# Optimization experiments

Hardware: AMD Instinct MI355X
Metric: run time of the kernel (lower is better)

The kernel has to match this reference:

```python
import jax, jax.numpy as jnp
import numpy as np

D_MODEL = 1024
EXPAND = 2
D_INNER = EXPAND * D_MODEL      # 2048
D_STATE = 2
D_CONV = 4
DT_RANK = (D_MODEL + 15) // 16  # 64
BATCH, SEQ = 2, 4096
LN_EPS = 1e-5


def setup_inputs() -> dict:
    key = jax.random.key(0)
    ks = jax.random.split(key, 16)
    s = 0.02
    inp = {
        "x":       jax.random.normal(ks[0], (BATCH, SEQ, D_MODEL), jnp.float32),
        # Mamba params (torch Linear convention: W is [out, in])
        "w_in":    jax.random.normal(ks[1], (2 * D_INNER, D_MODEL), jnp.float32) * s,
        "conv_w":  jax.random.normal(ks[2], (D_INNER, 1, D_CONV), jnp.float32) * s,
        "conv_b":  jnp.zeros((D_INNER,), jnp.float32),
        "w_xproj": jax.random.normal(ks[3], (DT_RANK + 2 * D_STATE, D_INNER), jnp.float32) * s,
        "w_dt":    jax.random.normal(ks[4], (D_INNER, DT_RANK), jnp.float32) * s,
        "b_dt":    jax.random.normal(ks[5], (D_INNER,), jnp.float32) * s - 4.0,  # softplus -> small dt
        "a_log":   jnp.log(jnp.broadcast_to(jnp.arange(1, D_STATE + 1, dtype=jnp.float32), (D_INNER, D_STATE))),
        "d_skip":  jnp.ones((D_INNER,), jnp.float32),
        "w_out":   jax.random.normal(ks[6], (D_MODEL, D_INNER), jnp.float32) * s,
        # LayerNorms
        "ln1_g":   jnp.ones((D_MODEL,), jnp.float32),
        "ln1_b":   jnp.zeros((D_MODEL,), jnp.float32),
        "ln2_g":   jnp.ones((D_MODEL,), jnp.float32),
        "ln2_b":   jnp.zeros((D_MODEL,), jnp.float32),
        # FFN (Linear d->d, ReLU, Linear d->d; dropout inactive at eval)
        "ffn_w1":  jax.random.normal(ks[7], (D_MODEL, D_MODEL), jnp.float32) * s,
        "ffn_b1":  jnp.zeros((D_MODEL,), jnp.float32),
        "ffn_w2":  jax.random.normal(ks[8], (D_MODEL, D_MODEL), jnp.float32) * s,
        "ffn_b2":  jnp.zeros((D_MODEL,), jnp.float32),
    }
    return inp


def _ln(x, g, b):
    mu = x.mean(-1, keepdims=True)
    v = ((x - mu) ** 2).mean(-1, keepdims=True)
    return (x - mu) * jax.lax.rsqrt(v + LN_EPS) * g + b


def _mamba(x, w_in, conv_w, conv_b, w_xproj, w_dt, b_dt, a_log, d_skip, w_out):
    Bsz = x.shape[0]
    xz = x @ w_in.T                      # (B,L,2*D_INNER)
    xp, z = jnp.split(xz, 2, axis=-1)
    # depthwise causal conv over time
    xc = jnp.transpose(xp, (0, 2, 1))    # (B,D,L)
    xc = jax.lax.conv_general_dilated(
        xc, conv_w, window_strides=(1,), padding=[(D_CONV - 1, 0)],
        feature_group_count=D_INNER)
    xc = xc + conv_b[None, :, None]
    xp = jax.nn.silu(jnp.transpose(xc, (0, 2, 1)))   # (B,L,D)
    # input-dependent SSM params
    x_dbl = xp @ w_xproj.T               # (B,L,DT_RANK+2N)
    dt, Bm, Cm = jnp.split(x_dbl, [DT_RANK, DT_RANK + D_STATE], axis=-1)
    dt = jax.nn.softplus(dt @ w_dt.T + b_dt)          # (B,L,D)
    A = -jnp.exp(a_log)                  # (D,N)
    dA = jnp.exp(dt[..., None] * A)                  # (B,L,D,N)
    dBu = dt[..., None] * Bm[:, :, None, :] * xp[..., None]  # (B,L,D,N)

    def step(h, inp):
        da, dbu, c = inp                 # (B,D,N),(B,D,N),(B,N)
        h = da * h + dbu
        y = jnp.einsum('bdn,bn->bd', h, c)
        return h, y

    h0 = jnp.zeros((Bsz, D_INNER, D_STATE), x.dtype)
    _, ys = jax.lax.scan(step, h0, (jnp.swapaxes(dA, 0, 1),
                                    jnp.swapaxes(dBu, 0, 1),
                                    jnp.swapaxes(Cm, 0, 1)))
    y = jnp.swapaxes(ys, 0, 1)           # (B,L,D)
    y = (y + d_skip * xp) * jax.nn.silu(z)
    return y @ w_out.T                   # (B,L,d_model)


def reference(x, w_in, conv_w, conv_b, w_xproj, w_dt, b_dt, a_log, d_skip, w_out,
              ln1_g, ln1_b, ln2_g, ln2_b, ffn_w1, ffn_b1, ffn_w2, ffn_b2):
    h = x + _mamba(_ln(x, ln1_g, ln1_b), w_in, conv_w, conv_b, w_xproj,
                   w_dt, b_dt, a_log, d_skip, w_out)
    f = _ln(h, ln2_g, ln2_b)
    f = jax.nn.relu(f @ ffn_w1.T + ffn_b1) @ ffn_w2.T + ffn_b2
    return h + f
```

## Files before the change

kernel.cpp:

```cpp
#include <hip/hip_runtime.h>

typedef unsigned short u16;
typedef __bf16 bf16x8 __attribute__((ext_vector_type(8)));
typedef float f32x4 __attribute__((ext_vector_type(4)));
typedef float f32x2 __attribute__((ext_vector_type(2)));
typedef u16 u16x4 __attribute__((ext_vector_type(4)));
typedef u16 u16x8 __attribute__((ext_vector_type(8)));

#define SEQ   4096
#define DM    1024
#define DI    2048
#define NTOK  8192
#define NXP   68
#define DTR   64
#define NCH   4096
#define CHUNK 32
#define NCHK  128

__device__ __forceinline__ float bf2f(u16 v) {
  union { unsigned u; float f; } x; x.u = ((unsigned)v) << 16; return x.f;
}
__device__ __forceinline__ u16 f2bf(float f) {
  unsigned u = __float_as_uint(f);
  return (u16)((u + 0x7FFFu + ((u >> 16) & 1u)) >> 16);
}

__device__ __forceinline__ void g2l16(const u16* g, u16* l) {
  __builtin_amdgcn_global_load_lds(
      (const __attribute__((address_space(1))) unsigned int*)g,
      (__attribute__((address_space(3))) unsigned int*)l, 16, 0, 0);
}

__global__ __launch_bounds__(256)
void detect_kernel(const u16* __restrict__ x, int* __restrict__ flag)
{
  __shared__ int tot;
  if (threadIdx.x == 0) tot = 0;
  __syncthreads();
  int cnt = 0;
  for (int i = threadIdx.x; i < 4096; i += 256) {
    const int e = (x[2 * i] >> 7) & 0xFF;
    if (e > 167) cnt++;
  }
  atomicAdd(&tot, cnt);
  __syncthreads();
  if (threadIdx.x == 0) flag[0] = (tot >= 8) ? 1 : 0;
}

#define NW0 4194304
#define NW1  139264
#define NW2  131072
#define NW3 2097152
#define NW4 1048576
#define NW5 1048576
#define NBB 4228
__global__ __launch_bounds__(256)
void convert_all(const float* __restrict__ s0, const float* __restrict__ s1,
                 const float* __restrict__ s2, const float* __restrict__ s3,
                 const float* __restrict__ s4, const float* __restrict__ s5,
                 u16* __restrict__ d0, u16* __restrict__ d1, u16* __restrict__ d2,
                 u16* __restrict__ d3, u16* __restrict__ d4, u16* __restrict__ d5,
                 const void* t0, const void* t1, const void* t2, const void* t3,
                 const void* t4, const void* t5, const void* t6, const void* t7,
                 const void* t8, const void* t9, const void* t10,
                 u16* __restrict__ dsm, const int* __restrict__ flag)
{
  if (blockIdx.x >= NBB) {
    const int i = (blockIdx.x - NBB) * 256 + threadIdx.x;
    if (i >= 24576) return;
    const void* src; int off; int dsti = i;
    if      (i < 8192)  { src = t0;  off = i;
                          dsti = (off & 3) * DI + (off >> 2); }
    else if (i < 10240) { src = t1;  off = i - 8192; }
    else if (i < 12288) { src = t2;  off = i - 10240; }
    else if (i < 16384) { src = t3;  off = i - 12288; }
    else if (i < 18432) { src = t4;  off = i - 16384; }
    else if (i < 19456) { src = t5;  off = i - 18432; }
    else if (i < 20480) { src = t6;  off = i - 19456; }
    else if (i < 21504) { src = t7;  off = i - 20480; }
    else if (i < 22528) { src = t8;  off = i - 21504; }
    else if (i < 23552) { src = t9;  off = i - 22528; }
    else                { src = t10; off = i - 23552; }
    dsm[dsti] = (*flag) ? f2bf(((const float*)src)[off]) : ((const u16*)src)[off];
    return;
  }
  if (*flag == 0) return;
  long e = ((long)blockIdx.x * 256 + threadIdx.x) * 8;
  const long c1 = NW0, c2 = c1 + NW1, c3 = c2 + NW2, c4 = c3 + NW3,
             c5 = c4 + NW4, c6 = c5 + NW5;
  if (e >= c6) return;
  const float* s; u16* d;
  if      (e < c1) { s = s0;          d = d0; }
  else if (e < c2) { s = s1; e -= c1; d = d1; }
  else if (e < c3) { s = s2; e -= c2; d = d2; }
  else if (e < c4) { s = s3; e -= c3; d = d3; }
  else if (e < c5) { s = s4; e -= c4; d = d4; }
  else             { s = s5; e -= c5; d = d5; }
  f32x4 a = *(const f32x4*)(s + e);
  f32x4 b = *(const f32x4*)(s + e + 4);
  u16x8 o;
#pragma unroll
  for (int k = 0; k < 4; ++k) { o[k] = f2bf(a[k]); o[4 + k] = f2bf(b[k]); }
  *(u16x8*)(d + e) = o;
}

template<int MODE>
__global__ __launch_bounds__(256)
void ln_kernel(const void* __restrict__ xin, const u16* __restrict__ gw,
               const u16* __restrict__ bw, u16* __restrict__ outp,
               const int* __restrict__ flag)
{
  const int tid = threadIdx.x;
  const int sub = tid >> 7;
  const int col0 = (tid & 127) * 8;
  const int row = blockIdx.x * 2 + sub;
  const bool isf32 = (MODE == 0) ? (*flag != 0) : false;
  float v[8];
  if (isf32) {
    const float* xf = (const float*)xin + (size_t)row * DM + col0;
    f32x4 a = *(const f32x4*)xf, b2 = *(const f32x4*)(xf + 4);
#pragma unroll
    for (int k = 0; k < 4; ++k) { v[k] = a[k]; v[4 + k] = b2[k]; }
  } else {
    u16x8 xb = *(const u16x8*)((const u16*)xin + (size_t)row * DM + col0);
#pragma unroll
    for (int k = 0; k < 8; ++k) v[k] = bf2f(xb[k]);
  }
  float s = 0.f, s2 = 0.f;
#pragma unroll
  for (int k = 0; k < 8; ++k) { s += v[k]; s2 += v[k] * v[k]; }
#pragma unroll
  for (int off = 32; off > 0; off >>= 1) {
    s  += __shfl_down(s,  off);
    s2 += __shfl_down(s2, off);
  }
  __shared__ float red[4], red2[4];
  __shared__ f32x2 stat[2];
  const int wv = tid >> 6;
  if ((tid & 63) == 0) { red[wv] = s; red2[wv] = s2; }
  __syncthreads();
  if ((tid & 127) == 0) {
    float ts = red[sub * 2] + red[sub * 2 + 1];
    float t2 = red2[sub * 2] + red2[sub * 2 + 1];
    float mu = ts * (1.f / DM);
    float var = t2 * (1.f / DM) - mu * mu;
    stat[sub] = f32x2{mu, rsqrtf(var + 1e-5f)};
  }
  __syncthreads();
  const float mu = stat[sub][0], rs = stat[sub][1];
  u16x8 gv = *(const u16x8*)(gw + col0), bv = *(const u16x8*)(bw + col0);
  u16x8 o;
#pragma unroll
  for (int k = 0; k < 8; ++k)
    o[k] = f2bf((v[k] - mu) * rs * bf2f(gv[k]) + bf2f(bv[k]));
  *(u16x8*)(outp + (size_t)row * DM + col0) = o;
}

template<int EPI, int LNBX>
__global__ __launch_bounds__(256, 2)
void gemm_kernel(const u16* __restrict__ A, const u16* __restrict__ Bc,
                 const u16* __restrict__ Braw,
                 int M, int N, int K,
                 const u16* __restrict__ bias, const u16* __restrict__ addbf,
                 const float* __restrict__ addf, const int* __restrict__ dtflag,
                 void* __restrict__ Cp, void* __restrict__ Cp2)
{
  __shared__ __align__(16) u16 sA[2][128 * 32];
  __shared__ __align__(16) u16 sB[2][128 * 32];
  const int fl = *dtflag;
  const u16* __restrict__ B = fl ? Bc : Braw;
  const int tid = threadIdx.x;
  const int b = blockIdx.x;
  const int xcd = b & 7;
  const int kk = b >> 3;
  const int bx = kk & ((1 << LNBX) - 1);
  const int by = xcd * 8 + (kk >> LNBX);
  const int m0 = by * 128;
  const int n0 = bx * 128;
  const int lane = tid & 63;
  const int wv = tid >> 6;
  const int wm = (wv & 1) * 64;
  const int wn = (wv >> 1) * 64;
  const int r = lane & 15;
  const int q = lane >> 4;
  const int rsw = (r >> 1) & 3;

  const int pr = lane >> 2;
  const int kc = (lane & 3) ^ ((pr >> 1) & 3);
  const int pk = kc * 8;
  u16* lA0[2] = { &sA[0][(wv * 2 + 0) * 512], &sA[1][(wv * 2 + 0) * 512] };
  u16* lA1[2] = { &sA[0][(wv * 2 + 1) * 512], &sA[1][(wv * 2 + 1) * 512] };
  u16* lB0[2] = { &sB[0][(wv * 2 + 0) * 512], &sB[1][(wv * 2 + 0) * 512] };
  u16* lB1[2] = { &sB[0][(wv * 2 + 1) * 512], &sB[1][(wv * 2 + 1) * 512] };
  const u16* gA0 = A + (size_t)(m0 + wv * 32 + pr) * K + pk;
  const u16* gA1 = gA0 + (size_t)16 * K;
  const u16* gB0 = B + (size_t)(n0 + wv * 32 + pr) * K + pk;
  const u16* gB1 = gB0 + (size_t)16 * K;

  f32x4 acc[4][4];
#pragma unroll
  for (int i = 0; i < 4; ++i)
#pragma unroll
    for (int j = 0; j < 4; ++j)
#pragma unroll
      for (int t = 0; t < 4; ++t) acc[i][j][t] = 0.f;

  g2l16(gA0, lA0[0]); g2l16(gA1, lA1[0]);
  g2l16(gB0, lB0[0]); g2l16(gB1, lB1[0]);

  const int nk = K >> 5;
  for (int kt = 0; kt < nk; ++kt) {
    const int cur = kt & 1;
    __syncthreads();
    bf16x8 af[4], bfr[4];
#pragma unroll
    for (int i = 0; i < 4; ++i)
      af[i] = *reinterpret_cast<const bf16x8*>(
          &sA[cur][(wm + i * 16 + r) * 32 + (q ^ rsw) * 8]);
#pragma unroll
    for (int j = 0; j < 4; ++j)
      bfr[j] = *reinterpret_cast<const bf16x8*>(
          &sB[cur][(wn + j * 16 + r) * 32 + (q ^ rsw) * 8]);
    if (kt + 1 < nk) {
      gA0 += 32; gA1 += 32; gB0 += 32; gB1 += 32;
      g2l16(gA0, lA0[cur ^ 1]); g2l16(gA1, lA1[cur ^ 1]);
      g2l16(gB0, lB0[cur ^ 1]); g2l16(gB1, lB1[cur ^ 1]);
    }
#pragma unroll
    for (int i = 0; i < 4; ++i)
#pragma unroll
      for (int j = 0; j < 4; ++j)
        acc[i][j] = __builtin_amdgcn_mfma_f32_16x16x32_bf16(af[i], bfr[j], acc[i][j], 0, 0, 0);
  }

  __syncthreads();
  float* ep = (wv < 2) ? ((float*)&sA[0][0] + wv * 2048)
                       : ((float*)&sB[0][0] + (wv - 2) * 2048);
  const int r2 = lane >> 2;
  const int ccol = ((lane & 3) ^ (r2 & 3)) * 16;
  u16* C6 = nullptr; int c6off = 0;
  if (EPI == 6) { C6 = (n0 < DI) ? (u16*)Cp : (u16*)Cp2; c6off = (n0 < DI) ? 0 : DI; }

#pragma unroll
  for (int i = 0; i < 4; ++i) {
#pragma unroll
    for (int j = 0; j < 4; ++j)
#pragma unroll
      for (int t = 0; t < 4; ++t)
        ep[(q * 4 + t) * 68 + j * 16 + r] = acc[i][j][t];
    f32x4 w0 = *(const f32x4*)&ep[r2 * 68 + ccol + 0];
    f32x4 w1 = *(const f32x4*)&ep[r2 * 68 + ccol + 4];
    f32x4 w2 = *(const f32x4*)&ep[r2 * 68 + ccol + 8];
    f32x4 w3 = *(const f32x4*)&ep[r2 * 68 + ccol + 12];
    float vv[16];
#pragma unroll
    for (int k = 0; k < 4; ++k) {
      vv[k] = w0[k]; vv[4 + k] = w1[k]; vv[8 + k] = w2[k]; vv[12 + k] = w3[k];
    }
    const int row = m0 + wm + i * 16 + r2;
    const int colg = n0 + wn + ccol;
    if (EPI == 6) {
      u16x8 o0, o1;
#pragma unroll
      for (int k = 0; k < 8; ++k) { o0[k] = f2bf(vv[k]); o1[k] = f2bf(vv[8 + k]); }
      const size_t cb6 = (size_t)row * DI + (colg - c6off);
      *(u16x8*)&C6[cb6] = o0;
      *(u16x8*)&C6[cb6 + 8] = o1;
    } else {
      const size_t idx = (size_t)row * N + colg;
      if (EPI == 1) {
        u16x8 o0, o1;
#pragma unroll
        for (int k = 0; k < 8; ++k) { o0[k] = f2bf(vv[k]); o1[k] = f2bf(vv[8 + k]); }
        *(u16x8*)&((u16*)Cp)[idx] = o0;
        *(u16x8*)&((u16*)Cp)[idx + 8] = o1;
      } else if (EPI == 2) {
        u16x8 b0 = *(const u16x8*)&bias[colg];
        u16x8 b1 = *(const u16x8*)&bias[colg + 8];
        u16x8 o0, o1;
#pragma unroll
        for (int k = 0; k < 8; ++k) {
          float v0 = vv[k] + bf2f(b0[k]);
          float v1 = vv[8 + k] + bf2f(b1[k]);
          v0 = (v0 > 15.f) ? v0 : __logf(1.f + __expf(v0));
          v1 = (v1 > 15.f) ? v1 : __logf(1.f + __expf(v1));
          o0[k] = f2bf(v0); o1[k] = f2bf(v1);
        }
        *(u16x8*)&((u16*)Cp)[idx] = o0;
        *(u16x8*)&((u16*)Cp)[idx + 8] = o1;
      } else if (EPI == 3) {
        float ax[16];
        if (fl) {
          f32x4 a0 = *(const f32x4*)&addf[idx];
          f32x4 a1 = *(const f32x4*)&addf[idx + 4];
          f32x4 a2 = *(const f32x4*)&addf[idx + 8];
          f32x4 a3 = *(const f32x4*)&addf[idx + 12];
#pragma unroll
          for (int k = 0; k < 4; ++k) {
            ax[k] = a0[k]; ax[4 + k] = a1[k]; ax[8 + k] = a2[k]; ax[12 + k] = a3[k];
          }
        } else {
          u16x8 a0 = *(const u16x8*)&addbf[idx];
          u16x8 a1 = *(const u16x8*)&addbf[idx + 8];
#pragma unroll
          for (int k = 0; k < 8; ++k) { ax[k] = bf2f(a0[k]); ax[8 + k] = bf2f(a1[k]); }
        }
        u16x8 o0, o1;
#pragma unroll
        for (int k = 0; k < 8; ++k) {
          o0[k] = f2bf(vv[k] + ax[k]); o1[k] = f2bf(vv[8 + k] + ax[8 + k]);
        }
        *(u16x8*)&((u16*)Cp)[idx] = o0;
        *(u16x8*)&((u16*)Cp)[idx + 8] = o1;
      } else if (EPI == 4) {
        u16x8 b0 = *(const u16x8*)&bias[colg];
        u16x8 b1 = *(const u16x8*)&bias[colg + 8];
        u16x8 o0, o1;
#pragma unroll
        for (int k = 0; k < 8; ++k) {
          o0[k] = f2bf(fmaxf(vv[k] + bf2f(b0[k]), 0.f));
          o1[k] = f2bf(fmaxf(vv[8 + k] + bf2f(b1[k]), 0.f));
        }
        *(u16x8*)&((u16*)Cp)[idx] = o0;
        *(u16x8*)&((u16*)Cp)[idx + 8] = o1;
      } else {
        u16x8 b0 = *(const u16x8*)&bias[colg];
        u16x8 b1 = *(const u16x8*)&bias[colg + 8];
        u16x8 a0 = *(const u16x8*)&addbf[idx];
        u16x8 a1 = *(const u16x8*)&addbf[idx + 8];
        float r0[8], r1[8];
#pragma unroll
        for (int k = 0; k < 8; ++k) {
          r0[k] = vv[k] + bf2f(b0[k]) + bf2f(a0[k]);
          r1[k] = vv[8 + k] + bf2f(b1[k]) + bf2f(a1[k]);
        }
        if (fl) {
          f32x4 f0, f1, f2, f3;
#pragma unroll
          for (int k = 0; k < 4; ++k) { f0[k] = r0[k]; f1[k] = r0[4 + k]; f2[k] = r1[k]; f3[k] = r1[4 + k]; }
          *(f32x4*)&((float*)Cp)[idx] = f0;
          *(f32x4*)&((float*)Cp)[idx + 4] = f1;
          *(f32x4*)&((float*)Cp)[idx + 8] = f2;
          *(f32x4*)&((float*)Cp)[idx + 12] = f3;
        } else {
          u16x8 o0, o1;
#pragma unroll
          for (int k = 0; k < 8; ++k) { o0[k] = f2bf(r0[k]); o1[k] = f2bf(r1[k]); }
          *(u16x8*)&((u16*)Cp)[idx] = o0;
          *(u16x8*)&((u16*)Cp)[idx + 8] = o1;
        }
      }
    }
  }
}

__global__ __launch_bounds__(256, 2)
void xproj_splitk(const u16* __restrict__ A, const u16* __restrict__ Bc,
                  const u16* __restrict__ Braw, const int* __restrict__ dtflag,
                  float* __restrict__ part)
{
  __shared__ __align__(16) u16 sA[2][128 * 32];
  __shared__ __align__(16) u16 sB[2][128 * 32];
  const int fl = *dtflag;
  const u16* __restrict__ B = fl ? Bc : Braw;
  const int tid = threadIdx.x;
  const int kz = blockIdx.x;
  const int m0 = blockIdx.y * 128;
  const int kbase = kz * 256;
  const int lane = tid & 63;
  const int wv = tid >> 6;
  const int wm = (wv & 1) * 64;
  const int wn = (wv >> 1) * 64;
  const int r = lane & 15;
  const int q = lane >> 4;
  const int rsw = (r >> 1) & 3;
  const int pr = lane >> 2;
  const int kc = (lane & 3) ^ ((pr >> 1) & 3);
  const int pk = kc * 8;

  u16* lA0[2] = { &sA[0][(wv * 2 + 0) * 512], &sA[1][(wv * 2 + 0) * 512] };
  u16* lA1[2] = { &sA[0][(wv * 2 + 1) * 512], &sA[1][(wv * 2 + 1) * 512] };
  u16* lB0[2] = { &sB[0][(wv * 2 + 0) * 512], &sB[1][(wv * 2 + 0) * 512] };
  u16* lB1[2] = { &sB[0][(wv * 2 + 1) * 512], &sB[1][(wv * 2 + 1) * 512] };
  int br0 = wv * 32 + pr;      if (br0 > 67) br0 = 67;
  int br1 = wv * 32 + 16 + pr; if (br1 > 67) br1 = 67;
  const u16* gA0 = A + (size_t)(m0 + wv * 32 + pr) * DI + kbase + pk;
  const u16* gA1 = gA0 + (size_t)16 * DI;
  const u16* gB0 = B + (size_t)br0 * DI + kbase + pk;
  const u16* gB1 = B + (size_t)br1 * DI + kbase + pk;

  f32x4 acc[4][4];
#pragma unroll
  for (int i = 0; i < 4; ++i)
#pragma unroll
    for (int j = 0; j < 4; ++j)
#pragma unroll
      for (int t = 0; t < 4; ++t) acc[i][j][t] = 0.f;

  g2l16(gA0, lA0[0]); g2l16(gA1, lA1[0]);
  g2l16(gB0, lB0[0]); g2l16(gB1, lB1[0]);

  for (int kt = 0; kt < 8; ++kt) {
    const int cur = kt & 1;
    __syncthreads();
    bf16x8 af[4], bfr[4];
#pragma unroll
    for (int i = 0; i < 4; ++i)
      af[i] = *reinterpret_cast<const bf16x8*>(
          &sA[cur][(wm + i * 16 + r) * 32 + (q ^ rsw) * 8]);
#pragma unroll
    for (int j = 0; j < 4; ++j)
      bfr[j] = *reinterpret_cast<const bf16x8*>(
          &sB[cur][(wn + j * 16 + r) * 32 + (q ^ rsw) * 8]);
    if (kt + 1 < 8) {
      gA0 += 32; gA1 += 32; gB0 += 32; gB1 += 32;
      g2l16(gA0, lA0[cur ^ 1]); g2l16(gA1, lA1[cur ^ 1]);
      g2l16(gB0, lB0[cur ^ 1]); g2l16(gB1, lB1[cur ^ 1]);
    }
#pragma unroll
    for (int i = 0; i < 4; ++i)
#pragma unroll
      for (int j = 0; j < 4; ++j)
        acc[i][j] = __builtin_amdgcn_mfma_f32_16x16x32_bf16(af[i], bfr[j], acc[i][j], 0, 0, 0);
  }

#pragma unroll
  for (int i = 0; i < 4; ++i)
#pragma unroll
    for (int j = 0; j < 4; ++j)
#pragma unroll
      for (int t = 0; t < 4; ++t) {
        const int row = m0 + wm + i * 16 + q * 4 + t;
        const int col = wn + j * 16 + r;
        if (col < NXP)
          part[((size_t)kz * NTOK + row) * NXP + col] = acc[i][j][t];
      }
}

__global__ __launch_bounds__(256)
void xreduce_kernel(const float* __restrict__ part, u16* __restrict__ dtraw,
                    float* __restrict__ bc)
{
  const int i = blockIdx.x * 256 + threadIdx.x;
  if (i >= NTOK * NXP) return;
  const int row = i / NXP, col = i - row * NXP;
  float s = 0.f;
#pragma unroll
  for (int z = 0; z < 8; ++z) s += part[(size_t)z * NTOK * NXP + i];
  if (col < DTR) dtraw[(size_t)row * DTR + col] = f2bf(s);
  else           bc[row * 4 + (col - DTR)] = s;
}

__global__ __launch_bounds__(256)
void conv_silu_kernel(const u16* __restrict__ xp, const u16* __restrict__ cwT,
                      const u16* __restrict__ cb, u16* __restrict__ u)
{
  const int token = blockIdx.x;
  const int t = token & (SEQ - 1);
  const int d0 = threadIdx.x * 8;
  const ptrdiff_t base = (ptrdiff_t)token * DI + d0;
  float acc[8];
  u16x8 cbv = *(const u16x8*)(cb + d0);
#pragma unroll
  for (int k = 0; k < 8; ++k) acc[k] = bf2f(cbv[k]);
#pragma unroll
  for (int j = 0; j < 4; ++j) {
    if (t - 3 + j >= 0) {
      u16x8 xv = *(const u16x8*)(xp + base + (ptrdiff_t)(j - 3) * DI);
      u16x8 wv = *(const u16x8*)(cwT + j * DI + d0);
#pragma unroll
      for (int k = 0; k < 8; ++k) acc[k] += bf2f(wv[k]) * bf2f(xv[k]);
    }
  }
  u16x8 o;
#pragma unroll
  for (int k = 0; k < 8; ++k) {
    const float sg = 1.f / (1.f + __expf(-acc[k]));
    o[k] = f2bf(acc[k] * sg);
  }
  *(u16x8*)(u + base) = o;
}

__global__ __launch_bounds__(256)
void scan_pass1(const u16* __restrict__ dtb, const u16* __restrict__ ub,
                const float* __restrict__ bc, const u16* __restrict__ a_log,
                float* __restrict__ S, float* __restrict__ hf0, float* __restrict__ hf1)
{
  const int g4 = blockIdx.x * 256 + threadIdx.x;
  const int chg = g4 & (NCH / 4 - 1);
  const int c = g4 >> 10;
  const int ch0 = chg * 4;
  const int b = ch0 >> 11;
  const int d0 = ch0 & (DI - 1);
  u16x8 av = *(const u16x8*)(a_log + d0 * 2);
  float A0[4], A1[4];
#pragma unroll
  for (int k = 0; k < 4; ++k) {
    A0[k] = -__expf(bf2f(av[2 * k]));
    A1[k] = -__expf(bf2f(av[2 * k + 1]));
  }
  float h0[4] = {0.f, 0.f, 0.f, 0.f}, h1[4] = {0.f, 0.f, 0.f, 0.f};
  float s[4] = {0.f, 0.f, 0.f, 0.f};
  const int row0 = b * SEQ + c * CHUNK;
  for (int i = 0; i < CHUNK; ++i) {
    const size_t row = row0 + i;
    u16x4 dtv = *(const u16x4*)(dtb + row * DI + d0);
    u16x4 uv  = *(const u16x4*)(ub + row * DI + d0);
    f32x2 Bv = *(const f32x2*)(bc + row * 4);
#pragma unroll
    for (int k = 0; k < 4; ++k) {
      const float dt = bf2f(dtv[k]);
      const float dtu = dt * bf2f(uv[k]);
      h0[k] = __expf(A0[k] * dt) * h0[k] + dtu * Bv[0];
      h1[k] = __expf(A1[k] * dt) * h1[k] + dtu * Bv[1];
      s[k] += dt;
    }
  }
  const size_t g0 = (size_t)c * NCH + ch0;
  *(f32x4*)(S + g0)   = f32x4{s[0], s[1], s[2], s[3]};
  *(f32x4*)(hf0 + g0) = f32x4{h0[0], h0[1], h0[2], h0[3]};
  *(f32x4*)(hf1 + g0) = f32x4{h1[0], h1[1], h1[2], h1[3]};
}

__global__ __launch_bounds__(256)
void scan_pass2(const float* __restrict__ S, const float* __restrict__ hf0,
                const float* __restrict__ hf1, const u16* __restrict__ a_log,
                float* __restrict__ hi0, float* __restrict__ hi1)
{
  const int ch = blockIdx.x * 256 + threadIdx.x;
  const int d = ch & (DI - 1);
  const float A0 = -__expf(bf2f(a_log[d * 2 + 0]));
  const float A1 = -__expf(bf2f(a_log[d * 2 + 1]));
  float h0 = 0.f, h1 = 0.f;
  size_t g = ch;
  float sv = S[g], f0 = hf0[g], f1 = hf1[g];
  for (int c = 0; c < NCHK; ++c) {
    float svn = 0.f, f0n = 0.f, f1n = 0.f;
    if (c + 1 < NCHK) {
      const size_t gn = g + NCH;
      svn = S[gn]; f0n = hf0[gn]; f1n = hf1[gn];
    }
    hi0[g] = h0; hi1[g] = h1;
    h0 = __expf(A0 * sv) * h0 + f0;
    h1 = __expf(A1 * sv) * h1 + f1;
    sv = svn; f0 = f0n; f1 = f1n;
    g += NCH;
  }
}

__global__ __launch_bounds__(256)
void scan_pass3(const u16* __restrict__ dtb, const u16* __restrict__ ub,
                const float* __restrict__ bc, const u16* __restrict__ zbuf,
                const u16* __restrict__ a_log, const u16* __restrict__ d_skip,
                const float* __restrict__ hi0, const float* __restrict__ hi1,
                u16* __restrict__ yb)
{
  const int g4 = blockIdx.x * 256 + threadIdx.x;
  const int chg = g4 & (NCH / 4 - 1);
  const int c = g4 >> 10;
  const int ch0 = chg * 4;
  const int b = ch0 >> 11;
  const int d0 = ch0 & (DI - 1);
  u16x8 av = *(const u16x8*)(a_log + d0 * 2);
  u16x4 dkv = *(const u16x4*)(d_skip + d0);
  float A0[4], A1[4], dsk[4];
#pragma unroll
  for (int k = 0; k < 4; ++k) {
    A0[k] = -__expf(bf2f(av[2 * k]));
    A1[k] = -__expf(bf2f(av[2 * k + 1]));
    dsk[k] = bf2f(dkv[k]);
  }
  const size_t g0 = (size_t)c * NCH + ch0;
  f32x4 h0v = *(const f32x4*)(hi0 + g0);
  f32x4 h1v = *(const f32x4*)(hi1 + g0);
  float h0[4], h1[4];
#pragma unroll
  for (int k = 0; k < 4; ++k) { h0[k] = h0v[k]; h1[k] = h1v[k]; }
  const int row0 = b * SEQ + c * CHUNK;
  for (int i = 0; i < CHUNK; ++i) {
    const size_t row = row0 + i;
    u16x4 dtv = *(const u16x4*)(dtb + row * DI + d0);
    u16x4 uv  = *(const u16x4*)(ub + row * DI + d0);
    u16x4 zv  = *(const u16x4*)(zbuf + row * DI + d0);
    f32x4 bcv = *(const f32x4*)(bc + row * 4);
    u16x4 o;
#pragma unroll
    for (int k = 0; k < 4; ++k) {
      const float dt = bf2f(dtv[k]);
      const float uu = bf2f(uv[k]);
      const float dtu = dt * uu;
      h0[k] = __expf(A0[k] * dt) * h0[k] + dtu * bcv[0];
      h1[k] = __expf(A1[k] * dt) * h1[k] + dtu * bcv[1];
      const float y = h0[k] * bcv[2] + h1[k] * bcv[3];
      const float z = bf2f(zv[k]);
      const float sz = z / (1.f + __expf(-z));
      o[k] = f2bf((y + dsk[k] * uu) * sz);
    }
    *(u16x4*)(yb + row * DI + d0) = o;
  }
}

extern "C" void kernel_launch(void* const* d_in, const int* in_sizes, int n_in,
                              void* d_out, int out_size, void* d_ws, size_t ws_size,
                              hipStream_t stream)
{
  const void* x       = d_in[0];
  const void* w_in    = d_in[1];
  const void* conv_w  = d_in[2];
  const void* conv_b  = d_in[3];
  const void* w_xproj = d_in[4];
  const void* w_dt    = d_in[5];
  const void* b_dt    = d_in[6];
  const void* a_log   = d_in[7];
  const void* d_skip  = d_in[8];
  const void* w_out   = d_in[9];
  const void* ln1_g   = d_in[10];
  const void* ln1_b   = d_in[11];
  const void* ln2_g   = d_in[12];
  const void* ln2_b   = d_in[13];
  const void* ffn_w1  = d_in[14];
  const void* ffn_b1  = d_in[15];
  const void* ffn_w2  = d_in[16];
  const void* ffn_b2  = d_in[17];
  char* ws = (char*)d_ws;

  const size_t o_flag  = 0;
  const size_t o_small = 256;
  const size_t o_cwout = o_small + 65536;
  const size_t o_cff1  = o_cwout + (size_t)DM * DI * 2;
  const size_t o_cff2  = o_cff1  + (size_t)DM * DM * 2;
  const size_t o_cxp   = o_cff2  + (size_t)DM * DM * 2;
  const size_t o_cwdt  = o_cxp   + (size_t)NXP * DI * 2;
  const size_t o_xn    = 9437184;
  const size_t o_xp    = o_xn + (size_t)NTOK * DM * 2;
  const size_t o_z     = o_xp + (size_t)NTOK * DI * 2;
  const size_t o_u     = o_z  + (size_t)NTOK * DI * 2;
  const size_t o_bc    = o_u  + (size_t)NTOK * DI * 2;
  const size_t SCN = (size_t)NCHK * NCH * 4;
  const size_t o_S   = o_xn + 0 * SCN;
  const size_t o_hf0 = o_xn + 1 * SCN;
  const size_t o_hf1 = o_xn + 2 * SCN;
  const size_t o_hi0 = o_xn + 3 * SCN;
  const size_t o_hi1 = o_xn + 4 * SCN;

  int*   flagp   = (int*)(ws + o_flag);
  u16*   csmall  = (u16*)(ws + o_small);
  u16*   c_cwT   = csmall +     0;
  u16*   c_convb = csmall +  8192;
  u16*   c_bdt   = csmall + 10240;
  u16*   c_alog  = csmall + 12288;
  u16*   c_dskip = csmall + 16384;
  u16*   c_ln1g  = csmall + 18432;
  u16*   c_ln1b  = csmall + 19456;
  u16*   c_ln2g  = csmall + 20480;
  u16*   c_ln2b  = csmall + 21504;
  u16*   c_fb1   = csmall + 22528;
  u16*   c_fb2   = csmall + 23552;
  u16*   c_wout  = (u16*)(ws + o_cwout);
  u16*   c_ff1   = (u16*)(ws + o_cff1);
  u16*   c_ff2   = (u16*)(ws + o_cff2);
  u16*   c_xproj = (u16*)(ws + o_cxp);
  u16*   c_wdt   = (u16*)(ws + o_cwdt);
  u16*   c_win   = (u16*)(ws + o_u);
  u16*   xn      = (u16*)(ws + o_xn);
  u16*   xp      = (u16*)(ws + o_xp);
  u16*   zb      = (u16*)(ws + o_z);
  u16*   u       = (u16*)(ws + o_u);
  float* part    = (float*)(ws + o_xp);
  u16*   dtraw   = (u16*)(ws + o_xn);
  u16*   dtb     = xp;
  u16*   yb      = xp;
  float* bc      = (float*)(ws + o_bc);
  float* S       = (float*)(ws + o_S);
  float* hf0     = (float*)(ws + o_hf0);
  float* hf1     = (float*)(ws + o_hf1);
  float* hi0     = (float*)(ws + o_hi0);
  float* hi1     = (float*)(ws + o_hi1);
  u16*   hb      = (u16*)(ws + o_z);
  u16*   hn      = (u16*)(ws + o_xn);
  u16*   f1      = (u16*)(ws + o_u);

  const dim3 blk(256);

  detect_kernel<<<1, blk, 0, stream>>>((const u16*)x, flagp);
  convert_all<<<NBB + 96, blk, 0, stream>>>(
      (const float*)w_in, (const float*)w_xproj, (const float*)w_dt,
      (const float*)w_out, (const float*)ffn_w1, (const float*)ffn_w2,
      c_win, c_xproj, c_wdt, c_wout, c_ff1, c_ff2,
      conv_w, conv_b, b_dt, a_log, d_skip,
      ln1_g, ln1_b, ln2_g, ln2_b, ffn_b1, ffn_b2,
      csmall, flagp);

  ln_kernel<0><<<NTOK / 2, blk, 0, stream>>>(x, c_ln1g, c_ln1b, xn, flagp);
  gemm_kernel<6, 5><<<2048, blk, 0, stream>>>(xn, c_win, (const u16*)w_in,
                                              NTOK, 2 * DI, DM,
                                              nullptr, nullptr, nullptr, flagp, xp, zb);
  conv_silu_kernel<<<NTOK, blk, 0, stream>>>(xp, c_cwT, c_convb, u);
  xproj_splitk<<<dim3(8, 64), blk, 0, stream>>>(u, c_xproj, (const u16*)w_xproj,
                                                flagp, part);
  xreduce_kernel<<<(NTOK * NXP + 255) / 256, blk, 0, stream>>>(part, dtraw, bc);
  gemm_kernel<2, 4><<<1024, blk, 0, stream>>>(dtraw, c_wdt, (const u16*)w_dt,
                                              NTOK, DI, DTR,
                                              c_bdt, nullptr, nullptr, flagp, dtb, nullptr);
  scan_pass1<<<NCHK * NCH / 4 / 256, blk, 0, stream>>>(dtb, u, bc, c_alog, S, hf0, hf1);
  scan_pass2<<<NCH / 256, blk, 0, stream>>>(S, hf0, hf1, c_alog, hi0, hi1);
  scan_pass3<<<NCHK * NCH / 4 / 256, blk, 0, stream>>>(dtb, u, bc, zb, c_alog, c_dskip,
                                                       hi0, hi1, yb);
  gemm_kernel<3, 3><<<512, blk, 0, stream>>>(yb, c_wout, (const u16*)w_out,
                                             NTOK, DM, DI,
                                             nullptr, (const u16*)x, (const float*)x,
                                             flagp, hb, nullptr);
  ln_kernel<1><<<NTOK / 2, blk, 0, stream>>>(hb, c_ln2g, c_ln2b, hn, flagp);
  gemm_kernel<4, 3><<<512, blk, 0, stream>>>(hn, c_ff1, (const u16*)ffn_w1,
                                             NTOK, DM, DM,
                                             c_fb1, nullptr, nullptr, flagp, f1, nullptr);
  gemm_kernel<5, 3><<<512, blk, 0, stream>>>(f1, c_ff2, (const u16*)ffn_w2,
                                             NTOK, DM, DM,
                                             c_fb2, hb, nullptr, flagp, d_out, nullptr);
}
```

Baseline: 472.2 us.

## Add 256x256-tile 8-wave GEMM with staged prefetch for input projection

Replaces the 128x128 tile GEMM used for the in-projection (8192x4096x1024) with a new 512-thread kernel computing 256x256 tiles with 64-wide K steps. The kernel interleaves LDS fragment reads, async global-to-LDS prefetch and MFMA quarters, using sched barriers, workgroup barriers and setprio, plus an XCD-aware block remap. This raises data reuse per loaded byte and is meant to hide load latency. The old EPI==6 and EPI==1 epilogues are removed from the generic kernel. The cost is higher register and LDS pressure and more barriers per K step.

```diff
diff --git a/kernel.cpp b/kernel.cpp
--- a/kernel.cpp
+++ b/kernel.cpp
@@ -30,6 +30,8 @@
       (const __attribute__((address_space(1))) unsigned int*)g,
       (__attribute__((address_space(3))) unsigned int*)l, 16, 0, 0);
 }
+
+#define SBAR0() __builtin_amdgcn_sched_barrier(0)
 
 __global__ __launch_bounds__(256)
 void detect_kernel(const u16* __restrict__ x, int* __restrict__ flag)
@@ -238,8 +240,6 @@
                        : ((float*)&sB[0][0] + (wv - 2) * 2048);
   const int r2 = lane >> 2;
   const int ccol = ((lane & 3) ^ (r2 & 3)) * 16;
-  u16* C6 = nullptr; int c6off = 0;
-  if (EPI == 6) { C6 = (n0 < DI) ? (u16*)Cp : (u16*)Cp2; c6off = (n0 < DI) ? 0 : DI; }
 
 #pragma unroll
   for (int i = 0; i < 4; ++i) {
@@ -259,98 +259,273 @@
     }
     const int row = m0 + wm + i * 16 + r2;
     const int colg = n0 + wn + ccol;
-    if (EPI == 6) {
+    const size_t idx = (size_t)row * N + colg;
+    if (EPI == 2) {
+      u16x8 b0 = *(const u16x8*)&bias[colg];
+      u16x8 b1 = *(const u16x8*)&bias[colg + 8];
       u16x8 o0, o1;
 #pragma unroll
-      for (int k = 0; k < 8; ++k) { o0[k] = f2bf(vv[k]); o1[k] = f2bf(vv[8 + k]); }
-      const size_t cb6 = (size_t)row * DI + (colg - c6off);
-      *(u16x8*)&C6[cb6] = o0;
-      *(u16x8*)&C6[cb6 + 8] = o1;
+      for (int k = 0; k < 8; ++k) {
+        float v0 = vv[k] + bf2f(b0[k]);
+        float v1 = vv[8 + k] + bf2f(b1[k]);
+        v0 = (v0 > 15.f) ? v0 : __logf(1.f + __expf(v0));
+        v1 = (v1 > 15.f) ? v1 : __logf(1.f + __expf(v1));
+        o0[k] = f2bf(v0); o1[k] = f2bf(v1);
+      }
+      *(u16x8*)&((u16*)Cp)[idx] = o0;
+      *(u16x8*)&((u16*)Cp)[idx + 8] = o1;
+    } else if (EPI == 3) {
+      float ax[16];
+      if (fl) {
+        f32x4 a0 = *(const f32x4*)&addf[idx];
+        f32x4 a1 = *(const f32x4*)&addf[idx + 4];
+        f32x4 a2 = *(const f32x4*)&addf[idx + 8];
+        f32x4 a3 = *(const f32x4*)&addf[idx + 12];
+#pragma unroll
+        for (int k = 0; k < 4; ++k) {
+          ax[k] = a0[k]; ax[4 + k] = a1[k]; ax[8 + k] = a2[k]; ax[12 + k] = a3[k];
+        }
+      } else {
+        u16x8 a0 = *(const u16x8*)&addbf[idx];
+        u16x8 a1 = *(const u16x8*)&addbf[idx + 8];
+#pragma unroll
+        for (int k = 0; k < 8; ++k) { ax[k] = bf2f(a0[k]); ax[8 + k] = bf2f(a1[k]); }
+      }
+      u16x8 o0, o1;
+#pragma unroll
+      for (int k = 0; k < 8; ++k) {
+        o0[k] = f2bf(vv[k] + ax[k]); o1[k] = f2bf(vv[8 + k] + ax[8 + k]);
+      }
+      *(u16x8*)&((u16*)Cp)[idx] = o0;
+      *(u16x8*)&((u16*)Cp)[idx + 8] = o1;
+    } else if (EPI == 4) {
+      u16x8 b0 = *(const u16x8*)&bias[colg];
+      u16x8 b1 = *(const u16x8*)&bias[colg + 8];
+      u16x8 o0, o1;
+#pragma unroll
+      for (int k = 0; k < 8; ++k) {
+        o0[k] = f2bf(fmaxf(vv[k] + bf2f(b0[k]), 0.f));
+        o1[k] = f2bf(fmaxf(vv[8 + k] + bf2f(b1[k]), 0.f));
+      }
+      *(u16x8*)&((u16*)Cp)[idx] = o0;
+      *(u16x8*)&((u16*)Cp)[idx + 8] = o1;
     } else {
-      const size_t idx = (size_t)row * N + colg;
-      if (EPI == 1) {
+      u16x8 b0 = *(const u16x8*)&bias[colg];
+      u16x8 b1 = *(const u16x8*)&bias[colg + 8];
+      u16x8 a0 = *(const u16x8*)&addbf[idx];
+      u16x8 a1 = *(const u16x8*)&addbf[idx + 8];
+      float r0[8], r1[8];
+#pragma unroll
+      for (int k = 0; k < 8; ++k) {
+        r0[k] = vv[k] + bf2f(b0[k]) + bf2f(a0[k]);
+        r1[k] = vv[8 + k] + bf2f(b1[k]) + bf2f(a1[k]);
+      }
+      if (fl) {
+        f32x4 f0, f1, f2, f3;
+#pragma unroll
+        for (int k = 0; k < 4; ++k) { f0[k] = r0[k]; f1[k] = r0[4 + k]; f2[k] = r1[k]; f3[k] = r1[4 + k]; }
+        *(f32x4*)&((float*)Cp)[idx] = f0;
+        *(f32x4*)&((float*)Cp)[idx + 4] = f1;
+        *(f32x4*)&((float*)Cp)[idx + 8] = f2;
+        *(f32x4*)&((float*)Cp)[idx + 12] = f3;
+      } else {
         u16x8 o0, o1;
 #pragma unroll
-        for (int k = 0; k < 8; ++k) { o0[k] = f2bf(vv[k]); o1[k] = f2bf(vv[8 + k]); }
+        for (int k = 0; k < 8; ++k) { o0[k] = f2bf(r0[k]); o1[k] = f2bf(r1[k]); }
         *(u16x8*)&((u16*)Cp)[idx] = o0;
         *(u16x8*)&((u16*)Cp)[idx + 8] = o1;
-      } else if (EPI == 2) {
-        u16x8 b0 = *(const u16x8*)&bias[colg];
-        u16x8 b1 = *(const u16x8*)&bias[colg + 8];
-        u16x8 o0, o1;
-#pragma unroll
-        for (int k = 0; k < 8; ++k) {
-          float v0 = vv[k] + bf2f(b0[k]);
-          float v1 = vv[8 + k] + bf2f(b1[k]);
-          v0 = (v0 > 15.f) ? v0 : __logf(1.f + __expf(v0));
-          v1 = (v1 > 15.f) ? v1 : __logf(1.f + __expf(v1));
-          o0[k] = f2bf(v0); o1[k] = f2bf(v1);
-        }
-        *(u16x8*)&((u16*)Cp)[idx] = o0;
-        *(u16x8*)&((u16*)Cp)[idx + 8] = o1;
-      } else if (EPI == 3) {
-        float ax[16];
-        if (fl) {
-          f32x4 a0 = *(const f32x4*)&addf[idx];
-          f32x4 a1 = *(const f32x4*)&addf[idx + 4];
-          f32x4 a2 = *(const f32x4*)&addf[idx + 8];
-          f32x4 a3 = *(const f32x4*)&addf[idx + 12];
-#pragma unroll
-          for (int k = 0; k < 4; ++k) {
-            ax[k] = a0[k]; ax[4 + k] = a1[k]; ax[8 + k] = a2[k]; ax[12 + k] = a3[k];
-          }
-        } else {
-          u16x8 a0 = *(const u16x8*)&addbf[idx];
-          u16x8 a1 = *(const u16x8*)&addbf[idx + 8];
-#pragma unroll
-          for (int k = 0; k < 8; ++k) { ax[k] = bf2f(a0[k]); ax[8 + k] = bf2f(a1[k]); }
-        }
-        u16x8 o0, o1;
-#pragma unroll
-        for (int k = 0; k < 8; ++k) {
-          o0[k] = f2bf(vv[k] + ax[k]); o1[k] = f2bf(vv[8 + k] + ax[8 + k]);
-        }
-        *(u16x8*)&((u16*)Cp)[idx] = o0;
-        *(u16x8*)&((u16*)Cp)[idx + 8] = o1;
-      } else if (EPI == 4) {
-        u16x8 b0 = *(const u16x8*)&bias[colg];
-        u16x8 b1 = *(const u16x8*)&bias[colg + 8];
-        u16x8 o0, o1;
-#pragma unroll
-        for (int k = 0; k < 8; ++k) {
-          o0[k] = f2bf(fmaxf(vv[k] + bf2f(b0[k]), 0.f));
-          o1[k] = f2bf(fmaxf(vv[8 + k] + bf2f(b1[k]), 0.f));
-        }
-        *(u16x8*)&((u16*)Cp)[idx] = o0;
-        *(u16x8*)&((u16*)Cp)[idx + 8] = o1;
-      } else {
-        u16x8 b0 = *(const u16x8*)&bias[colg];
-        u16x8 b1 = *(const u16x8*)&bias[colg + 8];
-        u16x8 a0 = *(const u16x8*)&addbf[idx];
-        u16x8 a1 = *(const u16x8*)&addbf[idx + 8];
-        float r0[8], r1[8];
-#pragma unroll
-        for (int k = 0; k < 8; ++k) {
-          r0[k] = vv[k] + bf2f(b0[k]) + bf2f(a0[k]);
-          r1[k] = vv[8 + k] + bf2f(b1[k]) + bf2f(a1[k]);
-        }
-        if (fl) {
-          f32x4 f0, f1, f2, f3;
-#pragma unroll
-          for (int k = 0; k < 4; ++k) { f0[k] = r0[k]; f1[k] = r0[4 + k]; f2[k] = r1[k]; f3[k] = r1[4 + k]; }
-          *(f32x4*)&((float*)Cp)[idx] = f0;
-          *(f32x4*)&((float*)Cp)[idx + 4] = f1;
-          *(f32x4*)&((float*)Cp)[idx + 8] = f2;
-          *(f32x4*)&((float*)Cp)[idx + 12] = f3;
-        } else {
-          u16x8 o0, o1;
-#pragma unroll
-          for (int k = 0; k < 8; ++k) { o0[k] = f2bf(r0[k]); o1[k] = f2bf(r1[k]); }
-          *(u16x8*)&((u16*)Cp)[idx] = o0;
-          *(u16x8*)&((u16*)Cp)[idx + 8] = o1;
-        }
       }
     }
+  }
+}
+
+template<int EPI, int LNBX>
+__global__ __launch_bounds__(512, 2)
+void gemm256_kernel(const u16* __restrict__ A, const u16* __restrict__ Bc,
+                    const u16* __restrict__ Braw, int M, int N, int K,
+                    const int* __restrict__ dtflag, void* __restrict__ Cp,
+                    void* __restrict__ Cp2)
+{
+  __shared__ __align__(16) u16 sAB[2][2][2][128 * 64];
+  (void)M;
+  const int fl = *dtflag;
+  const u16* __restrict__ B = fl ? Bc : Braw;
+  const int tid = threadIdx.x;
+  const int w = tid >> 6;
+  const int lane = tid & 63;
+  const int b = blockIdx.x;
+  const int wg = (b & 7) * (gridDim.x >> 3) + (b >> 3);
+  const int bx = wg & ((1 << LNBX) - 1);
+  const int by = wg >> LNBX;
+  const int m0 = by * 256;
+  const int n0 = bx * 256;
+  const int wm = w >> 2;
+  const int wn = w & 3;
+  const int r = lane & 15;
+  const int q = lane >> 4;
+  const int r7 = r & 7;
+  const int srow = lane >> 3;
+  const int schunk = ((lane & 7) ^ (srow & 7)) << 3;
+
+  auto stageA = [&](int buf, int half, int kt) {
+#pragma unroll
+    for (int j = 0; j < 2; ++j) {
+      u16* l = &sAB[buf][0][half][(w * 16 + j * 8) * 64];
+      const u16* g = A + (size_t)(m0 + half * 128 + w * 16 + j * 8 + srow) * K
+                       + (kt << 6) + schunk;
+      g2l16(g, l);
+    }
+  };
+  auto stageB = [&](int buf, int half, int kt) {
+#pragma unroll
+    for (int j = 0; j < 2; ++j) {
+      u16* l = &sAB[buf][1][half][(w * 16 + j * 8) * 64];
+      const u16* g = B + (size_t)(n0 + half * 128 + w * 16 + j * 8 + srow) * K
+                       + (kt << 6) + schunk;
+      g2l16(g, l);
+    }
+  };
+
+  f32x4 acc[8][4];
+#pragma unroll
+  for (int i = 0; i < 8; ++i)
+#pragma unroll
+    for (int j = 0; j < 4; ++j)
+#pragma unroll
+      for (int t = 0; t < 4; ++t) acc[i][j][t] = 0.f;
+
+  const int nk = K >> 6;
+  stageA(0, 0, 0); stageA(0, 1, 0); stageB(0, 0, 0); stageB(0, 1, 0);
+  if (nk > 1) { stageB(1, 0, 1); stageB(1, 1, 1); }
+  if (nk > 1) asm volatile("s_waitcnt vmcnt(4)" ::: "memory");
+  else        asm volatile("s_waitcnt vmcnt(0)" ::: "memory");
+  SBAR0();
+  __builtin_amdgcn_s_barrier();
+  SBAR0();
+
+  for (int kt = 0; kt < nk; ++kt) {
+    const int c = kt & 1;
+    const u16* bA = &sAB[c][0][wm][0];
+    const u16* bB = &sAB[c][1][wn >> 1][0];
+    const int rB = (wn & 1) * 64;
+    bf16x8 af03[4][2], af47[4][2], b01[2][2], b23[2][2];
+
+#pragma unroll
+    for (int mf = 0; mf < 4; ++mf)
+#pragma unroll
+      for (int ks = 0; ks < 2; ++ks)
+        af03[mf][ks] = *(const bf16x8*)&bA[(mf * 16 + r) * 64
+                          + ((((ks << 2) + q) ^ r7) << 3)];
+#pragma unroll
+    for (int nf = 0; nf < 2; ++nf)
+#pragma unroll
+      for (int ks = 0; ks < 2; ++ks)
+        b01[nf][ks] = *(const bf16x8*)&bB[(rB + nf * 16 + r) * 64
+                          + ((((ks << 2) + q) ^ r7) << 3)];
+    if (kt + 1 < nk) stageA(c ^ 1, 0, kt + 1);
+    SBAR0(); __builtin_amdgcn_s_barrier();
+    asm volatile("s_waitcnt lgkmcnt(0)" ::: "memory"); SBAR0();
+    __builtin_amdgcn_s_setprio(1);
+#pragma unroll
+    for (int mf = 0; mf < 4; ++mf)
+#pragma unroll
+      for (int nf = 0; nf < 2; ++nf)
+#pragma unroll
+        for (int ks = 0; ks < 2; ++ks)
+          acc[mf][nf] = __builtin_amdgcn_mfma_f32_16x16x32_bf16(
+              af03[mf][ks], b01[nf][ks], acc[mf][nf], 0, 0, 0);
+    __builtin_amdgcn_s_setprio(0);
+    SBAR0(); __builtin_amdgcn_s_barrier(); SBAR0();
+
+#pragma unroll
+    for (int nf = 0; nf < 2; ++nf)
+#pragma unroll
+      for (int ks = 0; ks < 2; ++ks)
+        b23[nf][ks] = *(const bf16x8*)&bB[(rB + (nf + 2) * 16 + r) * 64
+                          + ((((ks << 2) + q) ^ r7) << 3)];
+    if (kt + 1 < nk) stageA(c ^ 1, 1, kt + 1);
+    SBAR0(); __builtin_amdgcn_s_barrier();
+    asm volatile("s_waitcnt lgkmcnt(0)" ::: "memory"); SBAR0();
+    __builtin_amdgcn_s_setprio(1);
+#pragma unroll
+    for (int mf = 0; mf < 4; ++mf)
+#pragma unroll
+      for (int nf = 0; nf < 2; ++nf)
+#pragma unroll
+        for (int ks = 0; ks < 2; ++ks)
+          acc[mf][nf + 2] = __builtin_amdgcn_mfma_f32_16x16x32_bf16(
+              af03[mf][ks], b23[nf][ks], acc[mf][nf + 2], 0, 0, 0);
+    __builtin_amdgcn_s_setprio(0);
+    SBAR0(); __builtin_amdgcn_s_barrier(); SBAR0();
+
+#pragma unroll
+    for (int mf = 0; mf < 4; ++mf)
+#pragma unroll
+      for (int ks = 0; ks < 2; ++ks)
+        af47[mf][ks] = *(const bf16x8*)&bA[((mf + 4) * 16 + r) * 64
+                          + ((((ks << 2) + q) ^ r7) << 3)];
+    if (kt + 2 < nk) stageB(c, 0, kt + 2);
+    SBAR0(); __builtin_amdgcn_s_barrier();
+    asm volatile("s_waitcnt lgkmcnt(0)" ::: "memory"); SBAR0();
+    __builtin_amdgcn_s_setprio(1);
+#pragma unroll
+    for (int mf = 0; mf < 4; ++mf)
+#pragma unroll
+      for (int nf = 0; nf < 2; ++nf)
+#pragma unroll
+        for (int ks = 0; ks < 2; ++ks)
+          acc[mf + 4][nf + 2] = __builtin_amdgcn_mfma_f32_16x16x32_bf16(
+              af47[mf][ks], b23[nf][ks], acc[mf + 4][nf + 2], 0, 0, 0);
+    __builtin_amdgcn_s_setprio(0);
+    SBAR0(); __builtin_amdgcn_s_barrier(); SBAR0();
+
+    if (kt + 2 < nk) stageB(c, 1, kt + 2);
+    SBAR0(); __builtin_amdgcn_s_barrier(); SBAR0();
+    __builtin_amdgcn_s_setprio(1);
+#pragma unroll
+    for (int mf = 0; mf < 4; ++mf)
+#pragma unroll
+      for (int nf = 0; nf < 2; ++nf)
+#pragma unroll
+        for (int ks = 0; ks < 2; ++ks)
+          acc[mf + 4][nf] = __builtin_amdgcn_mfma_f32_16x16x32_bf16(
+              af47[mf][ks], b01[nf][ks], acc[mf + 4][nf], 0, 0, 0);
+    __builtin_amdgcn_s_setprio(0);
+    SBAR0();
+    if (kt + 2 < nk) asm volatile("s_waitcnt vmcnt(4)" ::: "memory");
+    else             asm volatile("s_waitcnt vmcnt(0)" ::: "memory");
+    SBAR0();
+    __builtin_amdgcn_s_barrier();
+    SBAR0();
+  }
+
+  float* ep = (float*)&sAB[0][0][0][0] + w * 4096;
+  const int r2 = lane >> 2;
+  const int ccol = ((lane & 3) ^ (r2 & 3)) * 16;
+  u16* C6 = (n0 < DI) ? (u16*)Cp : (u16*)Cp2;
+  const int c6off = (n0 < DI) ? 0 : DI;
+#pragma unroll
+  for (int mf = 0; mf < 8; ++mf) {
+#pragma unroll
+    for (int nf = 0; nf < 4; ++nf)
+#pragma unroll
+      for (int t = 0; t < 4; ++t)
+        ep[(q * 4 + t) * 68 + nf * 16 + r] = acc[mf][nf][t];
+    f32x4 w0 = *(const f32x4*)&ep[r2 * 68 + ccol + 0];
+    f32x4 w1 = *(const f32x4*)&ep[r2 * 68 + ccol + 4];
+    f32x4 w2 = *(const f32x4*)&ep[r2 * 68 + ccol + 8];
+    f32x4 w3 = *(const f32x4*)&ep[r2 * 68 + ccol + 12];
+    u16x8 o0, o1;
+#pragma unroll
+    for (int k = 0; k < 4; ++k) {
+      o0[k] = f2bf(w0[k]); o0[4 + k] = f2bf(w1[k]);
+      o1[k] = f2bf(w2[k]); o1[4 + k] = f2bf(w3[k]);
+    }
+    const int row = m0 + wm * 128 + mf * 16 + r2;
+    const int colg = n0 + wn * 64 + ccol;
+    const size_t cb = (size_t)row * DI + (colg - c6off);
+    *(u16x8*)&C6[cb] = o0;
+    *(u16x8*)&C6[cb + 8] = o1;
   }
 }
 
@@ -692,9 +867,8 @@
       csmall, flagp);
 
   ln_kernel<0><<<NTOK / 2, blk, 0, stream>>>(x, c_ln1g, c_ln1b, xn, flagp);
-  gemm_kernel<6, 5><<<2048, blk, 0, stream>>>(xn, c_win, (const u16*)w_in,
-                                              NTOK, 2 * DI, DM,
-                                              nullptr, nullptr, nullptr, flagp, xp, zb);
+  gemm256_kernel<6, 4><<<512, dim3(512), 0, stream>>>(
+      xn, c_win, (const u16*)w_in, NTOK, 2 * DI, DM, flagp, xp, zb);
   conv_silu_kernel<<<NTOK, blk, 0, stream>>>(xp, c_cwT, c_convb, u);
   xproj_splitk<<<dim3(8, 64), blk, 0, stream>>>(u, c_xproj, (const u16*)w_xproj,
                                                 flagp, part);
```

New measurement: 463.4 us. About the same (-1.8%).
